# Kernel optimization log

Measured on AMD Instinct MI355X. Metric: run time of the kernel, lower is better.

The kernel has to match this reference:

```python
import jax, jax.numpy as jnp
import numpy as np
from jax.ops import segment_sum, segment_max

N, E, F_IN, H1, H2, HEADS, OUT, G = 50000, 800000, 64, 64, 64, 4, 32, 500

def setup_inputs() -> dict:
    key = jax.random.key(0)
    ks = jax.random.split(key, 12)
    x = jax.random.normal(ks[0], (N, F_IN), dtype=jnp.float32)
    edge_index = jax.random.randint(ks[1], (2, E), 0, N, dtype=jnp.int64)
    batch = jnp.sort(jax.random.randint(ks[2], (N,), 0, G, dtype=jnp.int64))
    def glorot(k, shape):
        fan = shape[0] + shape[-1]
        return jax.random.uniform(k, shape, jnp.float32, -1.0, 1.0) * jnp.sqrt(6.0 / fan)
    return {
        "x": x,
        "edge_index": edge_index,
        "batch": batch,
        "gcn_W": glorot(ks[3], (F_IN, H1)),
        "gcn_b": jnp.zeros((H1,), jnp.float32),
        "gat_W": glorot(ks[4], (H1, HEADS * H2)),
        "att_src": glorot(ks[5], (HEADS, H2)),
        "att_dst": glorot(ks[6], (HEADS, H2)),
        "gat_b": jnp.zeros((HEADS * H2,), jnp.float32),
        "out_W": glorot(ks[7], (HEADS * H2, OUT)),
        "out_b": jnp.zeros((OUT,), jnp.float32),
    }

def reference(x, edge_index, batch, gcn_W, gcn_b, gat_W, att_src, att_dst, gat_b, out_W, out_b):
    n = x.shape[0]
    loop = jnp.arange(n)
    # edges with self-loops: src (j) -> dst (i), PyG convention
    src = jnp.concatenate([edge_index[0], loop])
    dst = jnp.concatenate([edge_index[1], loop])

    # ---- GCNConv: symmetric normalized scatter-add ----
    h = x @ gcn_W                                            # [N, H1]
    deg = segment_sum(jnp.ones_like(dst, dtype=h.dtype), dst, num_segments=n)
    dinv = jnp.where(deg > 0, jax.lax.rsqrt(deg), 0.0)       # deg^{-1/2}
    norm = dinv[src] * dinv[dst]                             # [E']
    h = segment_sum(norm[:, None] * h[src], dst, num_segments=n) + gcn_b
    h = jax.nn.relu(h)

    # ---- GATConv: per-edge attention + segment softmax over dst ----
    g = (h @ gat_W).reshape(n, HEADS, H2)                    # [N, H, C]
    a_s = jnp.einsum('nhc,hc->nh', g, att_src)               # [N, H]
    a_d = jnp.einsum('nhc,hc->nh', g, att_dst)
    e = jax.nn.leaky_relu(a_s[src] + a_d[dst], 0.2)          # [E', H]
    m = segment_max(e, dst, num_segments=n)                  # every node has a self-loop
    e = jnp.exp(e - m[dst])
    denom = segment_sum(e, dst, num_segments=n)
    alpha = e / denom[dst]                                   # [E', H]
    agg = segment_sum(alpha[:, :, None] * g[src], dst, num_segments=n)  # [N, H, C]
    z = jax.nn.relu(agg.reshape(n, HEADS * H2) + gat_b)

    # ---- global mean pool over graphs + output linear ----
    cnt = segment_sum(jnp.ones((n,), z.dtype), batch, num_segments=G)
    pooled = segment_sum(z, batch, num_segments=G) / jnp.maximum(cnt, 1.0)[:, None]
    return pooled @ out_W + out_b
```

## Files before the change

kernel.cpp:

```cpp
#include <hip/hip_runtime.h>
#include <math.h>

#define NN 50000
#define NE 800000
#define NEP (NE + NN)
#define NGRAPH 500
#define NOUT 32
#define NBLK 196

typedef _Float16 half4 __attribute__((ext_vector_type(4)));
typedef _Float16 half2v __attribute__((ext_vector_type(2)));

__device__ __forceinline__ float lrelu(float x) { return x > 0.f ? x : 0.2f * x; }
__device__ __forceinline__ half2v bch2(float f) { return __builtin_bit_cast(half2v, f); }

__device__ __forceinline__ unsigned fkey(float f) {
    unsigned b = __float_as_uint(f);
    return (b & 0x80000000u) ? ~b : (b | 0x80000000u);
}
__device__ __forceinline__ float funkey(unsigned k) {
    unsigned b = (k & 0x80000000u) ? (k & 0x7fffffffu) : ~k;
    return __uint_as_float(b);
}


__global__ void k_count(const int* __restrict__ dst, int* __restrict__ cnt,
                        int* __restrict__ pos) {
    int e = blockIdx.x * blockDim.x + threadIdx.x;
    if (e < NE) pos[e] = atomicAdd(&cnt[dst[e]], 1);
}

__global__ __launch_bounds__(256) void k_scan1(const int* __restrict__ cnt, int* __restrict__ bsum,
                                               float* __restrict__ pool, float* __restrict__ cnt_g) {
    __shared__ int buf[256];
    int gid = blockIdx.x * 256 + threadIdx.x;
    int v = (gid < NN) ? (cnt[gid] + 1) : 0;
    buf[threadIdx.x] = v;
    for (int j = gid; j < NGRAPH * 256; j += NBLK * 256) pool[j] = 0.f;
    if (gid < NGRAPH) cnt_g[gid] = 0.f;
    __syncthreads();
    for (int off = 128; off; off >>= 1) {
        if (threadIdx.x < off) buf[threadIdx.x] += buf[threadIdx.x + off];
        __syncthreads();
    }
    if (threadIdx.x == 0) bsum[blockIdx.x] = buf[0];
}

__global__ __launch_bounds__(256) void k_scan3(const int* __restrict__ cnt,
                                               const int* __restrict__ bsum,
                                               int* __restrict__ row_ptr,
                                               float* __restrict__ dinv,
                                               int* __restrict__ col) {
    __shared__ int sb[256];
    __shared__ int buf[256];
    int tid = threadIdx.x;
    int bv = (tid < NBLK) ? bsum[tid] : 0;
    sb[tid] = bv;
    __syncthreads();
    for (int off = 1; off < 256; off <<= 1) {
        int t = (tid >= off) ? sb[tid - off] : 0;
        __syncthreads();
        sb[tid] += t;
        __syncthreads();
    }
    int blockoff = (blockIdx.x == 0) ? 0 : sb[blockIdx.x - 1];
    int i = blockIdx.x * 256 + tid;
    int v = (i < NN) ? (cnt[i] + 1) : 0;
    buf[tid] = v;
    __syncthreads();
    for (int off = 1; off < 256; off <<= 1) {
        int t = (tid >= off) ? buf[tid - off] : 0;
        __syncthreads();
        buf[tid] += t;
        __syncthreads();
    }
    if (i < NN) {
        int rp = blockoff + buf[tid] - v;
        row_ptr[i] = rp;
        dinv[i] = rsqrtf((float)(cnt[i] + 1));
        col[rp] = i;
    }
    if (i == 0) row_ptr[NN] = NEP;
}

__global__ void k_fill(const int* __restrict__ src, const int* __restrict__ dst,
                       const int* __restrict__ row_ptr, const int* __restrict__ pos,
                       int* __restrict__ col) {
    int idx = blockIdx.x * blockDim.x + threadIdx.x;
    if (idx < NE) {
        int d = dst[idx];
        col[row_ptr[d] + 1 + pos[idx]] = src[idx];
    }
}


__global__ __launch_bounds__(256) void k_gemm64(const float* __restrict__ A,
                                                const float* __restrict__ B,
                                                const float* __restrict__ dinv,
                                                _Float16* __restrict__ C16, int n) {
    __shared__ float Bs[64 * 64];
    __shared__ float As[64 * 68];
    int tid = threadIdx.x;
    int rb = blockIdx.x * 64;
    for (int i = tid; i < 1024; i += 256) ((float4*)Bs)[i] = ((const float4*)B)[i];
    for (int i = tid; i < 1024; i += 256) {
        int r = i >> 4, c = i & 15;
        int row = rb + r; if (row >= n) row = n - 1;
        ((float4*)As)[r * 17 + c] = ((const float4*)A)[(size_t)row * 16 + c];
    }
    __syncthreads();
    int lane = tid & 63, wv = tid >> 6;
    int fl = lane & 15, sub = lane >> 4;
    int r0 = wv * 16 + sub * 4;
    const float4* Bs4 = (const float4*)Bs;
    float4 acc0 = {0,0,0,0}, acc1 = {0,0,0,0}, acc2 = {0,0,0,0}, acc3 = {0,0,0,0};
#pragma unroll 4
    for (int k = 0; k < 64; ++k) {
        float4 b4 = Bs4[k * 16 + fl];
        float a0 = As[(r0 + 0) * 68 + k];
        float a1 = As[(r0 + 1) * 68 + k];
        float a2 = As[(r0 + 2) * 68 + k];
        float a3 = As[(r0 + 3) * 68 + k];
        acc0.x += a0 * b4.x; acc0.y += a0 * b4.y; acc0.z += a0 * b4.z; acc0.w += a0 * b4.w;
        acc1.x += a1 * b4.x; acc1.y += a1 * b4.y; acc1.z += a1 * b4.z; acc1.w += a1 * b4.w;
        acc2.x += a2 * b4.x; acc2.y += a2 * b4.y; acc2.z += a2 * b4.z; acc2.w += a2 * b4.w;
        acc3.x += a3 * b4.x; acc3.y += a3 * b4.y; acc3.z += a3 * b4.z; acc3.w += a3 * b4.w;
    }
    int row = rb + r0;
    float d0 = dinv[row + 0 < n ? row + 0 : n - 1];
    float d1 = dinv[row + 1 < n ? row + 1 : n - 1];
    float d2 = dinv[row + 2 < n ? row + 2 : n - 1];
    float d3 = dinv[row + 3 < n ? row + 3 : n - 1];
    half4 h0, h1, h2, h3;
    h0.x=(_Float16)(acc0.x*d0); h0.y=(_Float16)(acc0.y*d0); h0.z=(_Float16)(acc0.z*d0); h0.w=(_Float16)(acc0.w*d0);
    h1.x=(_Float16)(acc1.x*d1); h1.y=(_Float16)(acc1.y*d1); h1.z=(_Float16)(acc1.z*d1); h1.w=(_Float16)(acc1.w*d1);
    h2.x=(_Float16)(acc2.x*d2); h2.y=(_Float16)(acc2.y*d2); h2.z=(_Float16)(acc2.z*d2); h2.w=(_Float16)(acc2.w*d2);
    h3.x=(_Float16)(acc3.x*d3); h3.y=(_Float16)(acc3.y*d3); h3.z=(_Float16)(acc3.z*d3); h3.w=(_Float16)(acc3.w*d3);
    if (row + 0 < n) ((half4*)(C16 + (size_t)(row + 0) * 64))[fl] = h0;
    if (row + 1 < n) ((half4*)(C16 + (size_t)(row + 1) * 64))[fl] = h1;
    if (row + 2 < n) ((half4*)(C16 + (size_t)(row + 2) * 64))[fl] = h2;
    if (row + 3 < n) ((half4*)(C16 + (size_t)(row + 3) * 64))[fl] = h3;
}


__global__ void k_uv(const float* __restrict__ gat_W, const float* __restrict__ att_src,
                     const float* __restrict__ att_dst, float* __restrict__ UV) {
    int idx = blockIdx.x * blockDim.x + threadIdx.x;
    if (idx >= 512) return;
    int f = idx >> 3, o = idx & 7, h = o & 3;
    const float* av = (o < 4) ? att_src : att_dst;
    float s = 0.f;
#pragma unroll 8
    for (int c = 0; c < 64; ++c) s += gat_W[f * 256 + h * 64 + c] * av[h * 64 + c];
    UV[idx] = s;
}


__global__ void k_w16t(const float* __restrict__ W, _Float16* __restrict__ W16T) {
    int idx = blockIdx.x * blockDim.x + threadIdx.x;
    if (idx >= 64 * 256) return;
    int c = idx >> 6, f = idx & 63;
    W16T[idx] = (_Float16)W[f * 256 + c];
}


__global__ __launch_bounds__(256) void k_gcn_agg(const _Float16* __restrict__ hxs16,
                                                 const int* __restrict__ row_ptr,
                                                 const int* __restrict__ col,
                                                 const float* __restrict__ dinv,
                                                 const float* __restrict__ bias,
                                                 const float* __restrict__ UV,
                                                 _Float16* __restrict__ h16,
                                                 float* __restrict__ a_s,
                                                 float* __restrict__ a_d) {
    int wid = (blockIdx.x * blockDim.x + threadIdx.x) >> 6;
    int lane = threadIdx.x & 63;
    if (wid >= NN) return;
    int slot = lane >> 4;
    int fl   = lane & 15;
    int s0 = row_ptr[wid], s1 = row_ptr[wid + 1];
    float di = dinv[wid];
    const half4* hx4 = (const half4*)hxs16;
    float ax = 0.f, ay = 0.f, az = 0.f, aw = 0.f;
    int k = s0 + slot;
    for (; k + 12 < s1; k += 16) {
        int i0 = col[k], i1 = col[k + 4], i2 = col[k + 8], i3 = col[k + 12];
        half4 v0 = hx4[(size_t)i0 * 16 + fl];
        half4 v1 = hx4[(size_t)i1 * 16 + fl];
        half4 v2 = hx4[(size_t)i2 * 16 + fl];
        half4 v3 = hx4[(size_t)i3 * 16 + fl];
        ax += ((float)v0.x + (float)v1.x) + ((float)v2.x + (float)v3.x);
        ay += ((float)v0.y + (float)v1.y) + ((float)v2.y + (float)v3.y);
        az += ((float)v0.z + (float)v1.z) + ((float)v2.z + (float)v3.z);
        aw += ((float)v0.w + (float)v1.w) + ((float)v2.w + (float)v3.w);
    }
    for (; k < s1; k += 4) {
        half4 v = hx4[(size_t)col[k] * 16 + fl];
        ax += (float)v.x; ay += (float)v.y;
        az += (float)v.z; aw += (float)v.w;
    }
    ax += __shfl_xor(ax, 16); ax += __shfl_xor(ax, 32);
    ay += __shfl_xor(ay, 16); ay += __shfl_xor(ay, 32);
    az += __shfl_xor(az, 16); az += __shfl_xor(az, 32);
    aw += __shfl_xor(aw, 16); aw += __shfl_xor(aw, 32);
    float4 bb = ((const float4*)bias)[fl];
    float zx = fmaxf(ax * di + bb.x, 0.f);
    float zy = fmaxf(ay * di + bb.y, 0.f);
    float zz = fmaxf(az * di + bb.z, 0.f);
    float zw = fmaxf(aw * di + bb.w, 0.f);
    if (slot == 0) {
        half4 z;
        z.x = (_Float16)zx; z.y = (_Float16)zy; z.z = (_Float16)zz; z.w = (_Float16)zw;
        ((half4*)(h16 + (size_t)wid * 64))[fl] = z;
    }
    int f0 = fl * 4;
    float ps = zx * UV[(f0 + 0) * 8 + slot] + zy * UV[(f0 + 1) * 8 + slot]
             + zz * UV[(f0 + 2) * 8 + slot] + zw * UV[(f0 + 3) * 8 + slot];
    float pd = zx * UV[(f0 + 0) * 8 + 4 + slot] + zy * UV[(f0 + 1) * 8 + 4 + slot]
             + zz * UV[(f0 + 2) * 8 + 4 + slot] + zw * UV[(f0 + 3) * 8 + 4 + slot];
    ps += __shfl_xor(ps, 1); pd += __shfl_xor(pd, 1);
    ps += __shfl_xor(ps, 2); pd += __shfl_xor(pd, 2);
    ps += __shfl_xor(ps, 4); pd += __shfl_xor(pd, 4);
    ps += __shfl_xor(ps, 8); pd += __shfl_xor(pd, 8);
    if (fl == 0) {
        a_s[wid * 4 + slot] = ps;
        a_d[wid * 4 + slot] = pd;
    }
}


__global__ __launch_bounds__(256) void k_gmax(const float* __restrict__ a_s,
                                              unsigned* __restrict__ gmaxU) {
    __shared__ unsigned sm[4];
    int tid = threadIdx.x;
    if (tid < 4) sm[tid] = 0u;
    __syncthreads();
    float mx = -1e30f, my = -1e30f, mz = -1e30f, mw = -1e30f;
    int stride = gridDim.x * 256;
    for (int n = blockIdx.x * 256 + tid; n < NN; n += stride) {
        float4 v = ((const float4*)a_s)[n];
        mx = fmaxf(mx, v.x); my = fmaxf(my, v.y);
        mz = fmaxf(mz, v.z); mw = fmaxf(mw, v.w);
    }
    atomicMax(&sm[0], fkey(mx)); atomicMax(&sm[1], fkey(my));
    atomicMax(&sm[2], fkey(mz)); atomicMax(&sm[3], fkey(mw));
    __syncthreads();
    if (tid < 4) atomicMax(&gmaxU[tid], sm[tid]);
}


__global__ __launch_bounds__(256) void k_gat_h(const _Float16* __restrict__ h16,
                                               const float* __restrict__ a_s,
                                               const float* __restrict__ a_d,
                                               const int* __restrict__ row_ptr,
                                               const int* __restrict__ col,
                                               const unsigned* __restrict__ gmaxU,
                                               _Float16* __restrict__ aggH) {
    int tid = threadIdx.x;
    int wv = tid >> 6, lane = tid & 63;
    int wid = blockIdx.x * 4 + wv;
    int slot = lane >> 4;
    int fl = lane & 15;

    int s0 = row_ptr[wid], s1 = row_ptr[wid + 1];
    float4 ad4 = ((const float4*)a_d)[wid];
    float M0 = lrelu(funkey(gmaxU[0]) + ad4.x);
    float M1 = lrelu(funkey(gmaxU[1]) + ad4.y);
    float M2 = lrelu(funkey(gmaxU[2]) + ad4.z);
    float M3 = lrelu(funkey(gmaxU[3]) + ad4.w);
    const half4* h4 = (const half4*)h16;
    const float4* as4 = (const float4*)a_s;

    float t0 = 1e-30f, t1 = 1e-30f, t2 = 1e-30f, t3 = 1e-30f;
    float4 A0 = {0,0,0,0}, A1 = {0,0,0,0}, A2 = {0,0,0,0}, A3 = {0,0,0,0};

    int k = s0 + slot;
    for (; k + 4 < s1; k += 8) {
        int ia = col[k], ib = col[k + 4];
        float4 ea = as4[ia];
        float4 eb = as4[ib];
        half4 va = h4[(size_t)ia * 16 + fl];
        half4 vb = h4[(size_t)ib * 16 + fl];
        float wa0 = __expf(lrelu(ea.x + ad4.x) - M0);
        float wa1 = __expf(lrelu(ea.y + ad4.y) - M1);
        float wa2 = __expf(lrelu(ea.z + ad4.z) - M2);
        float wa3 = __expf(lrelu(ea.w + ad4.w) - M3);
        float wb0 = __expf(lrelu(eb.x + ad4.x) - M0);
        float wb1 = __expf(lrelu(eb.y + ad4.y) - M1);
        float wb2 = __expf(lrelu(eb.z + ad4.z) - M2);
        float wb3 = __expf(lrelu(eb.w + ad4.w) - M3);
        t0 += wa0 + wb0; t1 += wa1 + wb1; t2 += wa2 + wb2; t3 += wa3 + wb3;
        float vax = (float)va.x, vay = (float)va.y, vaz = (float)va.z, vaw = (float)va.w;
        float vbx = (float)vb.x, vby = (float)vb.y, vbz = (float)vb.z, vbw = (float)vb.w;
        A0.x += wa0 * vax + wb0 * vbx; A0.y += wa0 * vay + wb0 * vby;
        A0.z += wa0 * vaz + wb0 * vbz; A0.w += wa0 * vaw + wb0 * vbw;
        A1.x += wa1 * vax + wb1 * vbx; A1.y += wa1 * vay + wb1 * vby;
        A1.z += wa1 * vaz + wb1 * vbz; A1.w += wa1 * vaw + wb1 * vbw;
        A2.x += wa2 * vax + wb2 * vbx; A2.y += wa2 * vay + wb2 * vby;
        A2.z += wa2 * vaz + wb2 * vbz; A2.w += wa2 * vaw + wb2 * vbw;
        A3.x += wa3 * vax + wb3 * vbx; A3.y += wa3 * vay + wb3 * vby;
        A3.z += wa3 * vaz + wb3 * vbz; A3.w += wa3 * vaw + wb3 * vbw;
    }
    if (k < s1) {
        int ia = col[k];
        float4 ea = as4[ia];
        half4 va = h4[(size_t)ia * 16 + fl];
        float wa0 = __expf(lrelu(ea.x + ad4.x) - M0);
        float wa1 = __expf(lrelu(ea.y + ad4.y) - M1);
        float wa2 = __expf(lrelu(ea.z + ad4.z) - M2);
        float wa3 = __expf(lrelu(ea.w + ad4.w) - M3);
        t0 += wa0; t1 += wa1; t2 += wa2; t3 += wa3;
        float vax = (float)va.x, vay = (float)va.y, vaz = (float)va.z, vaw = (float)va.w;
        A0.x += wa0 * vax; A0.y += wa0 * vay; A0.z += wa0 * vaz; A0.w += wa0 * vaw;
        A1.x += wa1 * vax; A1.y += wa1 * vay; A1.z += wa1 * vaz; A1.w += wa1 * vaw;
        A2.x += wa2 * vax; A2.y += wa2 * vay; A2.z += wa2 * vaz; A2.w += wa2 * vaw;
        A3.x += wa3 * vax; A3.y += wa3 * vay; A3.z += wa3 * vaz; A3.w += wa3 * vaw;
    }
#define REDX(x) x += __shfl_xor(x, 16); x += __shfl_xor(x, 32);
    REDX(t0) REDX(t1) REDX(t2) REDX(t3)
    REDX(A0.x) REDX(A0.y) REDX(A0.z) REDX(A0.w)
    REDX(A1.x) REDX(A1.y) REDX(A1.z) REDX(A1.w)
    REDX(A2.x) REDX(A2.y) REDX(A2.z) REDX(A2.w)
    REDX(A3.x) REDX(A3.y) REDX(A3.z) REDX(A3.w)
#undef REDX
    float rsel = slot == 0 ? t0 : slot == 1 ? t1 : slot == 2 ? t2 : t3;
    float4 Asel = slot == 0 ? A0 : slot == 1 ? A1 : slot == 2 ? A2 : A3;
    float r = 1.f / rsel;
    half4 o;
    o.x = (_Float16)(Asel.x * r); o.y = (_Float16)(Asel.y * r);
    o.z = (_Float16)(Asel.z * r); o.w = (_Float16)(Asel.w * r);
    ((half4*)(aggH + (size_t)wid * 256))[lane] = o;
}


__global__ __launch_bounds__(256) void k_post2(const _Float16* __restrict__ aggH,
                                               const _Float16* __restrict__ W16T,
                                               const float* __restrict__ gat_b,
                                               const int* __restrict__ batch,
                                               float* __restrict__ pool,
                                               float* __restrict__ cnt_g) {
    int tid = threadIdx.x;
    int lane = tid & 63;
    int wv = __builtin_amdgcn_readfirstlane(tid >> 6);
    int h = blockIdx.y;
    int c = h * 64 + lane;
    const float4* wp = (const float4*)(W16T + (size_t)c * 64);
    float4 Wb[8];
#pragma unroll
    for (int i = 0; i < 8; ++i) Wb[i] = wp[i];
    float gb = gat_b[c];

    int rbeg = (blockIdx.x * 4 + wv) * 32;
    int rend = rbeg + 32; if (rend > NN) rend = NN;

    float psum = 0.f;
    int curb = -1, rcnt = 0;
#pragma unroll 2
    for (int row = rbeg; row < rend; ++row) {
        int b = batch[row];
        if (b != curb) {
            if (curb >= 0) {
                atomicAdd(&pool[(size_t)curb * 256 + c], psum);
                if (h == 0 && lane == 0) atomicAdd(&cnt_g[curb], (float)rcnt);
            }
            psum = 0.f; rcnt = 0; curb = b;
        }
        const float4* ap = (const float4*)(aggH + (size_t)row * 256 + h * 64);
        float4 Ab[8];
#pragma unroll
        for (int i = 0; i < 8; ++i) Ab[i] = ap[i];
        float ac0 = 0.f, ac1 = 0.f, ac2 = 0.f, ac3 = 0.f;
#pragma unroll
        for (int i = 0; i < 8; ++i) {
            ac0 = __builtin_amdgcn_fdot2(bch2(Ab[i].x), bch2(Wb[i].x), ac0, false);
            ac1 = __builtin_amdgcn_fdot2(bch2(Ab[i].y), bch2(Wb[i].y), ac1, false);
            ac2 = __builtin_amdgcn_fdot2(bch2(Ab[i].z), bch2(Wb[i].z), ac2, false);
            ac3 = __builtin_amdgcn_fdot2(bch2(Ab[i].w), bch2(Wb[i].w), ac3, false);
        }
        float acc = (ac0 + ac1) + (ac2 + ac3);
        psum += fmaxf(acc + gb, 0.f);
        ++rcnt;
    }
    if (curb >= 0) {
        atomicAdd(&pool[(size_t)curb * 256 + c], psum);
        if (h == 0 && lane == 0) atomicAdd(&cnt_g[curb], (float)rcnt);
    }
}


__global__ void k_out(const float* __restrict__ pool, const float* __restrict__ cnt_g,
                      const float* __restrict__ W, const float* __restrict__ b,
                      float* __restrict__ out) {
    int idx = blockIdx.x * blockDim.x + threadIdx.x;
    if (idx >= NGRAPH * NOUT) return;
    int gg = idx >> 5, o = idx & 31;
    float c = cnt_g[gg];
    c = c > 1.f ? c : 1.f;
    float rinv = 1.f / c;
    const float* p = pool + (size_t)gg * 256;
    float acc = 0.f;
#pragma unroll 8
    for (int f = 0; f < 256; ++f) acc += p[f] * W[f * 32 + o];
    out[idx] = acc * rinv + b[o];
}


extern "C" void kernel_launch(void* const* d_in, const int* in_sizes, int n_in,
                              void* d_out, int out_size, void* d_ws, size_t ws_size,
                              hipStream_t stream) {
    const float* x       = (const float*)d_in[0];
    const int*   eidx    = (const int*)d_in[1];
    const int*   batch   = (const int*)d_in[2];
    const float* gcn_W   = (const float*)d_in[3];
    const float* gcn_b   = (const float*)d_in[4];
    const float* gat_W   = (const float*)d_in[5];
    const float* att_src = (const float*)d_in[6];
    const float* att_dst = (const float*)d_in[7];
    const float* gat_b   = (const float*)d_in[8];
    const float* out_W   = (const float*)d_in[9];
    const float* out_b   = (const float*)d_in[10];
    float* out = (float*)d_out;

    const int* src = eidx;
    const int* dst = eidx + NE;

    size_t off = 0;
    auto carve = [&](size_t bytes) -> char* {
        char* p = (char*)d_ws + off;
        off += (bytes + 255) & ~(size_t)255;
        return p;
    };
    int*      cnt     = (int*)carve(NN * sizeof(int));
    int*      pos     = (int*)carve((size_t)NE * sizeof(int));
    int*      row_ptr = (int*)carve((NN + 1) * sizeof(int));
    int*      bsum    = (int*)carve(256 * sizeof(int));
    int*      colb    = (int*)carve((size_t)NEP * sizeof(int));
    float*    dinv    = (float*)carve(NN * sizeof(float));
    _Float16* hx16    = (_Float16*)carve((size_t)NN * 64 * sizeof(_Float16));
    _Float16* h16     = (_Float16*)carve((size_t)NN * 64 * sizeof(_Float16));
    _Float16* aggH16  = (_Float16*)carve((size_t)NN * 256 * sizeof(_Float16));
    float*    a_s     = (float*)carve((size_t)NN * 4 * sizeof(float));
    float*    a_d     = (float*)carve((size_t)NN * 4 * sizeof(float));
    float*    UV      = (float*)carve(64 * 8 * sizeof(float));
    _Float16* W16T    = (_Float16*)carve(64 * 256 * sizeof(_Float16));
    unsigned* gmaxU   = (unsigned*)carve(4 * sizeof(unsigned));
    float*    pool    = (float*)carve((size_t)NGRAPH * 256 * sizeof(float));
    float*    cnt_g   = (float*)carve(NGRAPH * sizeof(float));

    hipMemsetAsync(cnt, 0, NN * sizeof(int), stream);
    hipMemsetAsync(gmaxU, 0, 4 * sizeof(unsigned), stream);

    k_count<<<(NE + 255) / 256, 256, 0, stream>>>(dst, cnt, pos);
    k_scan1<<<NBLK, 256, 0, stream>>>(cnt, bsum, pool, cnt_g);
    k_scan3<<<NBLK, 256, 0, stream>>>(cnt, bsum, row_ptr, dinv, colb);
    k_fill<<<(NE + 255) / 256, 256, 0, stream>>>(src, dst, row_ptr, pos, colb);

    k_uv<<<2, 256, 0, stream>>>(gat_W, att_src, att_dst, UV);
    k_w16t<<<64, 256, 0, stream>>>(gat_W, W16T);

    k_gemm64<<<(NN + 63) / 64, 256, 0, stream>>>(x, gcn_W, dinv, hx16, NN);
    k_gcn_agg<<<(NN * 64 + 255) / 256, 256, 0, stream>>>(hx16, row_ptr, colb, dinv, gcn_b,
                                                         UV, h16, a_s, a_d);

    k_gmax<<<128, 256, 0, stream>>>(a_s, gmaxU);
    k_gat_h<<<NN / 4, 256, 0, stream>>>(h16, a_s, a_d, row_ptr, colb, gmaxU, aggH16);

    k_post2<<<dim3(391, 4), 256, 0, stream>>>(aggH16, W16T, gat_b, batch, pool, cnt_g);

    k_out<<<(NGRAPH * NOUT + 255) / 256, 256, 0, stream>>>(pool, cnt_g, out_W, out_b, out);
}
```

Before: 317.5 us.

## Split node feature tables into halves to shrink gather working set

The GEMM output and the GCN hidden features are stored as two separate 32-wide fp16 halves instead of one 64-wide array. The GCN aggregation and GAT aggregation kernels each run twice, once per half, so every random gather touches a table half the size. The aim is to keep each pass's working set resident in cache for better hit rates. In exchange, the CSR indices and attention scores are re-read in each pass, launch count doubles, and a_s/a_d are built by a read-modify-write across the two GCN passes.

```diff
diff --git a/kernel.cpp b/kernel.cpp
--- a/kernel.cpp
+++ b/kernel.cpp
@@ -97,7 +97,8 @@
 __global__ __launch_bounds__(256) void k_gemm64(const float* __restrict__ A,
                                                 const float* __restrict__ B,
                                                 const float* __restrict__ dinv,
-                                                _Float16* __restrict__ C16, int n) {
+                                                _Float16* __restrict__ Clo,
+                                                _Float16* __restrict__ Chi, int n) {
     __shared__ float Bs[64 * 64];
     __shared__ float As[64 * 68];
     int tid = threadIdx.x;
@@ -136,10 +137,12 @@
     h1.x=(_Float16)(acc1.x*d1); h1.y=(_Float16)(acc1.y*d1); h1.z=(_Float16)(acc1.z*d1); h1.w=(_Float16)(acc1.w*d1);
     h2.x=(_Float16)(acc2.x*d2); h2.y=(_Float16)(acc2.y*d2); h2.z=(_Float16)(acc2.z*d2); h2.w=(_Float16)(acc2.w*d2);
     h3.x=(_Float16)(acc3.x*d3); h3.y=(_Float16)(acc3.y*d3); h3.z=(_Float16)(acc3.z*d3); h3.w=(_Float16)(acc3.w*d3);
-    if (row + 0 < n) ((half4*)(C16 + (size_t)(row + 0) * 64))[fl] = h0;
-    if (row + 1 < n) ((half4*)(C16 + (size_t)(row + 1) * 64))[fl] = h1;
-    if (row + 2 < n) ((half4*)(C16 + (size_t)(row + 2) * 64))[fl] = h2;
-    if (row + 3 < n) ((half4*)(C16 + (size_t)(row + 3) * 64))[fl] = h3;
+    _Float16* base = (fl < 8) ? Clo : Chi;
+    int fli = fl & 7;
+    if (row + 0 < n) ((half4*)(base + (size_t)(row + 0) * 32))[fli] = h0;
+    if (row + 1 < n) ((half4*)(base + (size_t)(row + 1) * 32))[fli] = h1;
+    if (row + 2 < n) ((half4*)(base + (size_t)(row + 2) * 32))[fli] = h2;
+    if (row + 3 < n) ((half4*)(base + (size_t)(row + 3) * 32))[fli] = h3;
 }
 
 
@@ -164,46 +167,45 @@
 }
 
 
-__global__ __launch_bounds__(256) void k_gcn_agg(const _Float16* __restrict__ hxs16,
-                                                 const int* __restrict__ row_ptr,
-                                                 const int* __restrict__ col,
-                                                 const float* __restrict__ dinv,
-                                                 const float* __restrict__ bias,
-                                                 const float* __restrict__ UV,
-                                                 _Float16* __restrict__ h16,
-                                                 float* __restrict__ a_s,
-                                                 float* __restrict__ a_d) {
+template<int HALF>
+__global__ __launch_bounds__(256) void k_gcn_h(const _Float16* __restrict__ hxh,
+                                               const int* __restrict__ row_ptr,
+                                               const int* __restrict__ col,
+                                               const float* __restrict__ dinv,
+                                               const float* __restrict__ bias,
+                                               const float* __restrict__ UV,
+                                               _Float16* __restrict__ hh,
+                                               float* __restrict__ a_s,
+                                               float* __restrict__ a_d) {
     int wid = (blockIdx.x * blockDim.x + threadIdx.x) >> 6;
     int lane = threadIdx.x & 63;
     if (wid >= NN) return;
-    int slot = lane >> 4;
-    int fl   = lane & 15;
+    int slot = lane >> 3;
+    int fl   = lane & 7;
     int s0 = row_ptr[wid], s1 = row_ptr[wid + 1];
     float di = dinv[wid];
-    const half4* hx4 = (const half4*)hxs16;
+    const half4* hx4 = (const half4*)hxh;
     float ax = 0.f, ay = 0.f, az = 0.f, aw = 0.f;
     int k = s0 + slot;
-    for (; k + 12 < s1; k += 16) {
-        int i0 = col[k], i1 = col[k + 4], i2 = col[k + 8], i3 = col[k + 12];
-        half4 v0 = hx4[(size_t)i0 * 16 + fl];
-        half4 v1 = hx4[(size_t)i1 * 16 + fl];
-        half4 v2 = hx4[(size_t)i2 * 16 + fl];
-        half4 v3 = hx4[(size_t)i3 * 16 + fl];
-        ax += ((float)v0.x + (float)v1.x) + ((float)v2.x + (float)v3.x);
-        ay += ((float)v0.y + (float)v1.y) + ((float)v2.y + (float)v3.y);
-        az += ((float)v0.z + (float)v1.z) + ((float)v2.z + (float)v3.z);
-        aw += ((float)v0.w + (float)v1.w) + ((float)v2.w + (float)v3.w);
-    }
-    for (; k < s1; k += 4) {
-        half4 v = hx4[(size_t)col[k] * 16 + fl];
+    for (; k + 8 < s1; k += 16) {
+        int i0 = col[k], i1 = col[k + 8];
+        half4 v0 = hx4[(size_t)i0 * 8 + fl];
+        half4 v1 = hx4[(size_t)i1 * 8 + fl];
+        ax += (float)v0.x + (float)v1.x;
+        ay += (float)v0.y + (float)v1.y;
+        az += (float)v0.z + (float)v1.z;
+        aw += (float)v0.w + (float)v1.w;
+    }
+    for (; k < s1; k += 8) {
+        half4 v = hx4[(size_t)col[k] * 8 + fl];
         ax += (float)v.x; ay += (float)v.y;
         az += (float)v.z; aw += (float)v.w;
     }
-    ax += __shfl_xor(ax, 16); ax += __shfl_xor(ax, 32);
-    ay += __shfl_xor(ay, 16); ay += __shfl_xor(ay, 32);
-    az += __shfl_xor(az, 16); az += __shfl_xor(az, 32);
-    aw += __shfl_xor(aw, 16); aw += __shfl_xor(aw, 32);
-    float4 bb = ((const float4*)bias)[fl];
+    ax += __shfl_xor(ax, 8); ax += __shfl_xor(ax, 16); ax += __shfl_xor(ax, 32);
+    ay += __shfl_xor(ay, 8); ay += __shfl_xor(ay, 16); ay += __shfl_xor(ay, 32);
+    az += __shfl_xor(az, 8); az += __shfl_xor(az, 16); az += __shfl_xor(az, 32);
+    aw += __shfl_xor(aw, 8); aw += __shfl_xor(aw, 16); aw += __shfl_xor(aw, 32);
+    float4 bb = ((const float4*)bias)[HALF * 8 + fl];
     float zx = fmaxf(ax * di + bb.x, 0.f);
     float zy = fmaxf(ay * di + bb.y, 0.f);
     float zz = fmaxf(az * di + bb.z, 0.f);
@@ -211,20 +213,19 @@
     if (slot == 0) {
         half4 z;
         z.x = (_Float16)zx; z.y = (_Float16)zy; z.z = (_Float16)zz; z.w = (_Float16)zw;
-        ((half4*)(h16 + (size_t)wid * 64))[fl] = z;
-    }
-    int f0 = fl * 4;
-    float ps = zx * UV[(f0 + 0) * 8 + slot] + zy * UV[(f0 + 1) * 8 + slot]
-             + zz * UV[(f0 + 2) * 8 + slot] + zw * UV[(f0 + 3) * 8 + slot];
-    float pd = zx * UV[(f0 + 0) * 8 + 4 + slot] + zy * UV[(f0 + 1) * 8 + 4 + slot]
-             + zz * UV[(f0 + 2) * 8 + 4 + slot] + zw * UV[(f0 + 3) * 8 + 4 + slot];
-    ps += __shfl_xor(ps, 1); pd += __shfl_xor(pd, 1);
-    ps += __shfl_xor(ps, 2); pd += __shfl_xor(pd, 2);
-    ps += __shfl_xor(ps, 4); pd += __shfl_xor(pd, 4);
-    ps += __shfl_xor(ps, 8); pd += __shfl_xor(pd, 8);
+        ((half4*)(hh + (size_t)wid * 32))[fl] = z;
+    }
+    int f0 = HALF * 32 + fl * 4;
+    float val = zx * UV[(f0 + 0) * 8 + slot] + zy * UV[(f0 + 1) * 8 + slot]
+              + zz * UV[(f0 + 2) * 8 + slot] + zw * UV[(f0 + 3) * 8 + slot];
+    val += __shfl_xor(val, 1);
+    val += __shfl_xor(val, 2);
+    val += __shfl_xor(val, 4);
     if (fl == 0) {
-        a_s[wid * 4 + slot] = ps;
-        a_d[wid * 4 + slot] = pd;
+        int idx = wid * 4 + (slot & 3);
+        float* dstp = (slot < 4) ? a_s : a_d;
+        if (HALF == 0) dstp[idx] = val;
+        else           dstp[idx] += val;
     }
 }
 
@@ -249,18 +250,19 @@
 }
 
 
-__global__ __launch_bounds__(256) void k_gat_h(const _Float16* __restrict__ h16,
-                                               const float* __restrict__ a_s,
-                                               const float* __restrict__ a_d,
-                                               const int* __restrict__ row_ptr,
-                                               const int* __restrict__ col,
-                                               const unsigned* __restrict__ gmaxU,
-                                               _Float16* __restrict__ aggH) {
+template<int HALF>
+__global__ __launch_bounds__(256) void k_gat_h2(const _Float16* __restrict__ hh,
+                                                const float* __restrict__ a_s,
+                                                const float* __restrict__ a_d,
+                                                const int* __restrict__ row_ptr,
+                                                const int* __restrict__ col,
+                                                const unsigned* __restrict__ gmaxU,
+                                                _Float16* __restrict__ aggH) {
     int tid = threadIdx.x;
     int wv = tid >> 6, lane = tid & 63;
     int wid = blockIdx.x * 4 + wv;
-    int slot = lane >> 4;
-    int fl = lane & 15;
+    int slot = lane >> 3;
+    int fl = lane & 7;
 
     int s0 = row_ptr[wid], s1 = row_ptr[wid + 1];
     float4 ad4 = ((const float4*)a_d)[wid];
@@ -268,19 +270,19 @@
     float M1 = lrelu(funkey(gmaxU[1]) + ad4.y);
     float M2 = lrelu(funkey(gmaxU[2]) + ad4.z);
     float M3 = lrelu(funkey(gmaxU[3]) + ad4.w);
-    const half4* h4 = (const half4*)h16;
+    const half4* h4 = (const half4*)hh;
     const float4* as4 = (const float4*)a_s;
 
     float t0 = 1e-30f, t1 = 1e-30f, t2 = 1e-30f, t3 = 1e-30f;
     float4 A0 = {0,0,0,0}, A1 = {0,0,0,0}, A2 = {0,0,0,0}, A3 = {0,0,0,0};
 
     int k = s0 + slot;
-    for (; k + 4 < s1; k += 8) {
-        int ia = col[k], ib = col[k + 4];
+    for (; k + 8 < s1; k += 16) {
+        int ia = col[k], ib = col[k + 8];
         float4 ea = as4[ia];
         float4 eb = as4[ib];
-        half4 va = h4[(size_t)ia * 16 + fl];
-        half4 vb = h4[(size_t)ib * 16 + fl];
+        half4 va = h4[(size_t)ia * 8 + fl];
+        half4 vb = h4[(size_t)ib * 8 + fl];
         float wa0 = __expf(lrelu(ea.x + ad4.x) - M0);
         float wa1 = __expf(lrelu(ea.y + ad4.y) - M1);
         float wa2 = __expf(lrelu(ea.z + ad4.z) - M2);
@@ -301,10 +303,10 @@
         A3.x += wa3 * vax + wb3 * vbx; A3.y += wa3 * vay + wb3 * vby;
         A3.z += wa3 * vaz + wb3 * vbz; A3.w += wa3 * vaw + wb3 * vbw;
     }
-    if (k < s1) {
+    for (; k < s1; k += 8) {
         int ia = col[k];
         float4 ea = as4[ia];
-        half4 va = h4[(size_t)ia * 16 + fl];
+        half4 va = h4[(size_t)ia * 8 + fl];
         float wa0 = __expf(lrelu(ea.x + ad4.x) - M0);
         float wa1 = __expf(lrelu(ea.y + ad4.y) - M1);
         float wa2 = __expf(lrelu(ea.z + ad4.z) - M2);
@@ -316,20 +318,22 @@
         A2.x += wa2 * vax; A2.y += wa2 * vay; A2.z += wa2 * vaz; A2.w += wa2 * vaw;
         A3.x += wa3 * vax; A3.y += wa3 * vay; A3.z += wa3 * vaz; A3.w += wa3 * vaw;
     }
-#define REDX(x) x += __shfl_xor(x, 16); x += __shfl_xor(x, 32);
+#define REDX(x) x += __shfl_xor(x, 8); x += __shfl_xor(x, 16); x += __shfl_xor(x, 32);
     REDX(t0) REDX(t1) REDX(t2) REDX(t3)
     REDX(A0.x) REDX(A0.y) REDX(A0.z) REDX(A0.w)
     REDX(A1.x) REDX(A1.y) REDX(A1.z) REDX(A1.w)
     REDX(A2.x) REDX(A2.y) REDX(A2.z) REDX(A2.w)
     REDX(A3.x) REDX(A3.y) REDX(A3.z) REDX(A3.w)
 #undef REDX
-    float rsel = slot == 0 ? t0 : slot == 1 ? t1 : slot == 2 ? t2 : t3;
-    float4 Asel = slot == 0 ? A0 : slot == 1 ? A1 : slot == 2 ? A2 : A3;
-    float r = 1.f / rsel;
-    half4 o;
-    o.x = (_Float16)(Asel.x * r); o.y = (_Float16)(Asel.y * r);
-    o.z = (_Float16)(Asel.z * r); o.w = (_Float16)(Asel.w * r);
-    ((half4*)(aggH + (size_t)wid * 256))[lane] = o;
+    if (slot < 4) {
+        float rsel = slot == 0 ? t0 : slot == 1 ? t1 : slot == 2 ? t2 : t3;
+        float4 Asel = slot == 0 ? A0 : slot == 1 ? A1 : slot == 2 ? A2 : A3;
+        float r = 1.f / rsel;
+        half4 o;
+        o.x = (_Float16)(Asel.x * r); o.y = (_Float16)(Asel.y * r);
+        o.z = (_Float16)(Asel.z * r); o.w = (_Float16)(Asel.w * r);
+        ((half4*)(aggH + (size_t)wid * 256 + slot * 64 + HALF * 32))[fl] = o;
+    }
 }
 
 
@@ -436,8 +440,10 @@
     int*      bsum    = (int*)carve(256 * sizeof(int));
     int*      colb    = (int*)carve((size_t)NEP * sizeof(int));
     float*    dinv    = (float*)carve(NN * sizeof(float));
-    _Float16* hx16    = (_Float16*)carve((size_t)NN * 64 * sizeof(_Float16));
-    _Float16* h16     = (_Float16*)carve((size_t)NN * 64 * sizeof(_Float16));
+    _Float16* hx_lo   = (_Float16*)carve((size_t)NN * 32 * sizeof(_Float16));
+    _Float16* hx_hi   = (_Float16*)carve((size_t)NN * 32 * sizeof(_Float16));
+    _Float16* h_lo    = (_Float16*)carve((size_t)NN * 32 * sizeof(_Float16));
+    _Float16* h_hi    = (_Float16*)carve((size_t)NN * 32 * sizeof(_Float16));
     _Float16* aggH16  = (_Float16*)carve((size_t)NN * 256 * sizeof(_Float16));
     float*    a_s     = (float*)carve((size_t)NN * 4 * sizeof(float));
     float*    a_d     = (float*)carve((size_t)NN * 4 * sizeof(float));
@@ -458,12 +464,15 @@
     k_uv<<<2, 256, 0, stream>>>(gat_W, att_src, att_dst, UV);
     k_w16t<<<64, 256, 0, stream>>>(gat_W, W16T);
 
-    k_gemm64<<<(NN + 63) / 64, 256, 0, stream>>>(x, gcn_W, dinv, hx16, NN);
-    k_gcn_agg<<<(NN * 64 + 255) / 256, 256, 0, stream>>>(hx16, row_ptr, colb, dinv, gcn_b,
-                                                         UV, h16, a_s, a_d);
+    k_gemm64<<<(NN + 63) / 64, 256, 0, stream>>>(x, gcn_W, dinv, hx_lo, hx_hi, NN);
+    k_gcn_h<0><<<NN / 4, 256, 0, stream>>>(hx_lo, row_ptr, colb, dinv, gcn_b, UV,
+                                           h_lo, a_s, a_d);
+    k_gcn_h<1><<<NN / 4, 256, 0, stream>>>(hx_hi, row_ptr, colb, dinv, gcn_b, UV,
+                                           h_hi, a_s, a_d);
 
     k_gmax<<<128, 256, 0, stream>>>(a_s, gmaxU);
-    k_gat_h<<<NN / 4, 256, 0, stream>>>(h16, a_s, a_d, row_ptr, colb, gmaxU, aggH16);
+    k_gat_h2<0><<<NN / 4, 256, 0, stream>>>(h_lo, a_s, a_d, row_ptr, colb, gmaxU, aggH16);
+    k_gat_h2<1><<<NN / 4, 256, 0, stream>>>(h_hi, a_s, a_d, row_ptr, colb, gmaxU, aggH16);
 
     k_post2<<<dim3(391, 4), 256, 0, stream>>>(aggH16, W16T, gat_b, batch, pool, cnt_g);
 
```

Result: slower. 338.8 us (+6.7%).
